# Performance work log

Measured on AMD Instinct MI355X. Metric: run time of the kernel, lower is better.

Reference implementation:

```python
import jax, jax.numpy as jnp
import numpy as np

ANGLE_DEG = 15.0  # matches init_kwargs angle; cv2 convention: positive = counter-clockwise


def setup_inputs() -> dict:
    key = jax.random.key(0)
    encode_image = jax.random.normal(key, (32, 3, 512, 512), dtype=jnp.float32)
    return {"encode_image": encode_image}


def _rotate(img, angle_deg):
    """Faithful jax version of cv2.getRotationMatrix2D + cv2.warpAffine
    (INTER_LINEAR, BORDER_CONSTANT=0, scale=1), batched over B,C.
    cv2.warpAffine inverts M, so dst(x,y) = src(R(-angle) @ (x-c, y-c) + c).
    """
    B, C, H, W = img.shape
    theta = jnp.float32(angle_deg * np.pi / 180.0)
    a, b = jnp.cos(theta), jnp.sin(theta)
    # original code uses center (H//2, W//2) with dsize (H, W); square images assumed
    cx = jnp.float32(H // 2)
    cy = jnp.float32(W // 2)
    X, Y = jnp.meshgrid(jnp.arange(W, dtype=jnp.float32),
                        jnp.arange(H, dtype=jnp.float32))  # [H, W] dst pixel coords
    # inverse rotation (R(angle)^-1 = R(-angle)) about center
    xs = a * (X - cx) - b * (Y - cy) + cx  # src column coord
    ys = b * (X - cx) + a * (Y - cy) + cy  # src row coord
    x0 = jnp.floor(xs)
    y0 = jnp.floor(ys)
    wx = xs - x0
    wy = ys - y0
    x0i = x0.astype(jnp.int32)
    y0i = y0.astype(jnp.int32)

    def tap(yi, xi, w):
        # per-tap border-constant-0 handling, as cv2 BORDER_CONSTANT does
        valid = (xi >= 0) & (xi <= W - 1) & (yi >= 0) & (yi <= H - 1)
        xc = jnp.clip(xi, 0, W - 1)
        yc = jnp.clip(yi, 0, H - 1)
        vals = img[:, :, yc, xc]  # gather -> [B, C, H, W]
        return vals * (w * valid)[None, None]

    out = (tap(y0i,     x0i,     (1 - wy) * (1 - wx))
         + tap(y0i,     x0i + 1, (1 - wy) * wx)
         + tap(y0i + 1, x0i,     wy * (1 - wx))
         + tap(y0i + 1, x0i + 1, wy * wx))
    return out


def reference(encode_image):
    return _rotate(encode_image, ANGLE_DEG)
```

## Files before the change

### kernel.cpp

```cpp
#include <hip/hip_runtime.h>


#define IMG_H 512
#define IMG_W 512
#define NPLANES 96
#define TSX 64
#define TSY 32
#define LROWS 50
#define LCOLS 76
#define GPR 19
#define NGROUPS_PAD 1024
#define LDS_FLOATS (NGROUPS_PAD * 4)

typedef __attribute__((address_space(1))) const float gfloat;
typedef __attribute__((address_space(3))) float sfloat;

template <bool MASKED>
__device__ __forceinline__ void compute_tile(const float* __restrict__ tile,
                                             float* __restrict__ dst,
                                             int X0, int Y0, int xs0a, int ys0,
                                             int t, float a, float b) {
    const int col4 = (t & 15) << 2;
    const int row_base = t >> 4;
#pragma unroll
    for (int rr = 0; rr < 2; ++rr) {
        const int y = Y0 + row_base + (rr << 4);
        const float fy = (float)y - 256.0f;
        const float bxs = -b * fy + 256.0f;
        const float bys =  a * fy + 256.0f;

        float o[4];
#pragma unroll
        for (int k = 0; k < 4; ++k) {
            const int x = X0 + col4 + k;
            const float fx = (float)x - 256.0f;
            const float xs = a * fx + bxs;
            const float ys = b * fx + bys;

            const float x0f = floorf(xs);
            const float y0f = floorf(ys);
            const float wx = xs - x0f;
            const float wy = ys - y0f;
            const int x0 = (int)x0f;
            const int y0 = (int)y0f;

            float w00 = (1.0f - wy) * (1.0f - wx);
            float w01 = (1.0f - wy) * wx;
            float w10 = wy * (1.0f - wx);
            float w11 = wy * wx;

            if (MASKED) {
                const float vx0 = ((unsigned)x0       < IMG_W) ? 1.0f : 0.0f;
                const float vx1 = ((unsigned)(x0 + 1) < IMG_W) ? 1.0f : 0.0f;
                const float vy0 = ((unsigned)y0       < IMG_H) ? 1.0f : 0.0f;
                const float vy1 = ((unsigned)(y0 + 1) < IMG_H) ? 1.0f : 0.0f;
                w00 *= vy0 * vx0;
                w01 *= vy0 * vx1;
                w10 *= vy1 * vx0;
                w11 *= vy1 * vx1;
            }

            const int lr = y0 - ys0;
            const int lc = x0 - xs0a;
            const float* __restrict__ p = &tile[lr * LCOLS + lc];
            const float v00 = p[0];
            const float v01 = p[1];
            const float v10 = p[LCOLS];
            const float v11 = p[LCOLS + 1];

            o[k] = v00 * w00 + v01 * w01 + v10 * w10 + v11 * w11;
        }
        *reinterpret_cast<float4*>(&dst[y * IMG_W + X0 + col4]) =
            make_float4(o[0], o[1], o[2], o[3]);
    }
}

__global__ __launch_bounds__(256, 8) void rot_kernel(const float* __restrict__ in,
                                                     float* __restrict__ out) {
    const float a = 0.96592582628906831f;
    const float b = 0.25881904510252074f;

    __shared__ float tile[LDS_FLOATS];

    const int blk = blockIdx.x;
    const int tx = blk & 7;
    const int ty = (blk >> 3) & 15;
    const int bc = blk >> 7;
    const int X0 = tx * TSX;
    const int Y0 = ty * TSY;

    const float fx_lo = (float)X0 - 256.0f;
    const float fy_lo = (float)Y0 - 256.0f;
    const float fy_hi = (float)(Y0 + (TSY - 1)) - 256.0f;
    const float xs_min = a * fx_lo + (-b * fy_hi + 256.0f);
    const float ys_min = b * fx_lo + ( a * fy_lo + 256.0f);
    const int xs0  = (int)floorf(xs_min);
    const int ys0  = (int)floorf(ys_min);
    const int xs0a = xs0 & ~3;

    const int t = threadIdx.x;
    const int wave = t >> 6;
    const int plane_base = bc * (IMG_H * IMG_W);
    const int total = NPLANES * IMG_H * IMG_W;

#pragma unroll
    for (int it = 0; it < NGROUPS_PAD / 256; ++it) {
        const int g = it * 256 + t;
        const int r = g / GPR;
        const int c4 = (g - r * GPR) << 2;
        int gidx = plane_base + (ys0 + r) * IMG_W + xs0a + c4;
        gidx = min(max(gidx, 0), total - 4);
        __builtin_amdgcn_global_load_lds(
            (gfloat*)(in + gidx),
            (sfloat*)&tile[(it * 256 + (wave << 6)) * 4],
            16, 0, 0);
    }
    __syncthreads();

    float* __restrict__ dst = out + (size_t)bc * (IMG_H * IMG_W);

    const bool interior = (xs0a >= 0) && (xs0a + LCOLS <= IMG_W) &&
                          (ys0 >= 0) && (ys0 + LROWS <= IMG_H);
    if (interior) {
        compute_tile<false>(tile, dst, X0, Y0, xs0a, ys0, t, a, b);
    } else {
        compute_tile<true>(tile, dst, X0, Y0, xs0a, ys0, t, a, b);
    }
}

extern "C" void kernel_launch(void* const* d_in, const int* in_sizes, int n_in,
                              void* d_out, int out_size, void* d_ws, size_t ws_size,
                              hipStream_t stream) {
    const float* in = (const float*)d_in[0];
    float* out = (float*)d_out;

    const int grid = NPLANES * (IMG_W / TSX) * (IMG_H / TSY);
    rot_kernel<<<grid, 256, 0, stream>>>(in, out);
}
```

Before: 174.0 us.

## Persistent blocks with double-buffered LDS prefetch of next tile

Replaces one-tile-per-block launch with 1024 persistent blocks that each process 12 consecutive tiles. The next tile's source window is loaded into a second LDS buffer with async global_load_lds while the current tile is computed, hiding load latency. Occupancy hint drops to 4 blocks/SM and LDS use doubles, which may reduce latency hiding across blocks. The __syncthreads before the store is relied on for the loads to complete, with no explicit wait on the async copies.

```diff
diff --git a/kernel.cpp b/kernel.cpp
--- a/kernel.cpp
+++ b/kernel.cpp
@@ -9,22 +9,46 @@
 #define LROWS 50
 #define LCOLS 76
 #define GPR 19
-#define NGROUPS_PAD 1024
-#define LDS_FLOATS (NGROUPS_PAD * 4)
+#define BUF_FLOATS 4096
+#define NBLOCKS 1024
+#define TPB 12
 
 typedef __attribute__((address_space(1))) const float gfloat;
 typedef __attribute__((address_space(3))) float sfloat;
 
+struct TileGeom {
+    int X0, Y0, xs0a, ys0, bc;
+    bool interior;
+};
+
+__device__ __forceinline__ TileGeom decode(int tl, float a, float b) {
+    TileGeom g;
+    g.bc = tl >> 7;
+    const int rem = tl & 127;
+    g.X0 = (rem & 7) * TSX;
+    g.Y0 = (rem >> 3) * TSY;
+    const float fx_lo = (float)g.X0 - 256.0f;
+    const float fy_lo = (float)g.Y0 - 256.0f;
+    const float fy_hi = (float)(g.Y0 + TSY - 1) - 256.0f;
+    const float xs_min = a * fx_lo + (-b * fy_hi + 256.0f);
+    const float ys_min = b * fx_lo + ( a * fy_lo + 256.0f);
+    const int xs0 = (int)floorf(xs_min);
+    g.ys0 = (int)floorf(ys_min);
+    g.xs0a = xs0 & ~3;
+    g.interior = (g.xs0a >= 0) && (g.xs0a + LCOLS <= IMG_W) &&
+                 (g.ys0 >= 0) && (g.ys0 + LROWS <= IMG_H);
+    return g;
+}
+
 template <bool MASKED>
-__device__ __forceinline__ void compute_tile(const float* __restrict__ tile,
-                                             float* __restrict__ dst,
-                                             int X0, int Y0, int xs0a, int ys0,
-                                             int t, float a, float b) {
+__device__ __forceinline__ void compute_px(const float* __restrict__ buf,
+                                           const TileGeom& G, int t,
+                                           float a, float b, float4 res[2]) {
     const int col4 = (t & 15) << 2;
     const int row_base = t >> 4;
 #pragma unroll
     for (int rr = 0; rr < 2; ++rr) {
-        const int y = Y0 + row_base + (rr << 4);
+        const int y = G.Y0 + row_base + (rr << 4);
         const float fy = (float)y - 256.0f;
         const float bxs = -b * fy + 256.0f;
         const float bys =  a * fy + 256.0f;
@@ -32,7 +56,7 @@
         float o[4];
 #pragma unroll
         for (int k = 0; k < 4; ++k) {
-            const int x = X0 + col4 + k;
+            const int x = G.X0 + col4 + k;
             const float fx = (float)x - 256.0f;
             const float xs = a * fx + bxs;
             const float ys = b * fx + bys;
@@ -60,9 +84,9 @@
                 w11 *= vy1 * vx1;
             }
 
-            const int lr = y0 - ys0;
-            const int lc = x0 - xs0a;
-            const float* __restrict__ p = &tile[lr * LCOLS + lc];
+            const int lr = y0 - G.ys0;
+            const int lc = x0 - G.xs0a;
+            const float* __restrict__ p = &buf[lr * LCOLS + lc];
             const float v00 = p[0];
             const float v01 = p[1];
             const float v10 = p[LCOLS];
@@ -70,61 +94,77 @@
 
             o[k] = v00 * w00 + v01 * w01 + v10 * w10 + v11 * w11;
         }
-        *reinterpret_cast<float4*>(&dst[y * IMG_W + X0 + col4]) =
-            make_float4(o[0], o[1], o[2], o[3]);
+        res[rr] = make_float4(o[0], o[1], o[2], o[3]);
     }
 }
 
-__global__ __launch_bounds__(256, 8) void rot_kernel(const float* __restrict__ in,
+__device__ __forceinline__ void store_px(float* __restrict__ out,
+                                         const TileGeom& G, int t,
+                                         const float4 res[2]) {
+    const int col4 = (t & 15) << 2;
+    const int row_base = t >> 4;
+    float* __restrict__ dst = out + (size_t)G.bc * (IMG_H * IMG_W);
+#pragma unroll
+    for (int rr = 0; rr < 2; ++rr) {
+        const int y = G.Y0 + row_base + (rr << 4);
+        *reinterpret_cast<float4*>(&dst[y * IMG_W + G.X0 + col4]) = res[rr];
+    }
+}
+
+__global__ __launch_bounds__(256, 4) void rot_kernel(const float* __restrict__ in,
                                                      float* __restrict__ out) {
     const float a = 0.96592582628906831f;
     const float b = 0.25881904510252074f;
 
-    __shared__ float tile[LDS_FLOATS];
-
-    const int blk = blockIdx.x;
-    const int tx = blk & 7;
-    const int ty = (blk >> 3) & 15;
-    const int bc = blk >> 7;
-    const int X0 = tx * TSX;
-    const int Y0 = ty * TSY;
-
-    const float fx_lo = (float)X0 - 256.0f;
-    const float fy_lo = (float)Y0 - 256.0f;
-    const float fy_hi = (float)(Y0 + (TSY - 1)) - 256.0f;
-    const float xs_min = a * fx_lo + (-b * fy_hi + 256.0f);
-    const float ys_min = b * fx_lo + ( a * fy_lo + 256.0f);
-    const int xs0  = (int)floorf(xs_min);
-    const int ys0  = (int)floorf(ys_min);
-    const int xs0a = xs0 & ~3;
+    __shared__ float tile[2][BUF_FLOATS];
 
     const int t = threadIdx.x;
     const int wave = t >> 6;
-    const int plane_base = bc * (IMG_H * IMG_W);
     const int total = NPLANES * IMG_H * IMG_W;
 
+    int gof[4], ldso[4];
 #pragma unroll
-    for (int it = 0; it < NGROUPS_PAD / 256; ++it) {
+    for (int it = 0; it < 4; ++it) {
         const int g = it * 256 + t;
         const int r = g / GPR;
         const int c4 = (g - r * GPR) << 2;
-        int gidx = plane_base + (ys0 + r) * IMG_W + xs0a + c4;
-        gidx = min(max(gidx, 0), total - 4);
-        __builtin_amdgcn_global_load_lds(
-            (gfloat*)(in + gidx),
-            (sfloat*)&tile[(it * 256 + (wave << 6)) * 4],
-            16, 0, 0);
+        gof[it] = r * IMG_W + c4;
+        ldso[it] = (it * 256 + (wave << 6)) * 4;
     }
+
+    auto stage = [&](const TileGeom& G, int p) {
+        const int base = G.bc * (IMG_H * IMG_W) + G.ys0 * IMG_W + G.xs0a;
+#pragma unroll
+        for (int it = 0; it < 4; ++it) {
+            int gidx = base + gof[it];
+            gidx = min(max(gidx, 0), total - 4);
+            __builtin_amdgcn_global_load_lds(
+                (gfloat*)(in + gidx), (sfloat*)&tile[p][ldso[it]], 16, 0, 0);
+        }
+    };
+
+    const int tile0 = blockIdx.x * TPB;
+
+    TileGeom G = decode(tile0, a, b);
+    stage(G, 0);
     __syncthreads();
 
-    float* __restrict__ dst = out + (size_t)bc * (IMG_H * IMG_W);
-
-    const bool interior = (xs0a >= 0) && (xs0a + LCOLS <= IMG_W) &&
-                          (ys0 >= 0) && (ys0 + LROWS <= IMG_H);
-    if (interior) {
-        compute_tile<false>(tile, dst, X0, Y0, xs0a, ys0, t, a, b);
-    } else {
-        compute_tile<true>(tile, dst, X0, Y0, xs0a, ys0, t, a, b);
+    float4 res[2];
+#pragma unroll 2
+    for (int i = 0; i < TPB; ++i) {
+        const int p = i & 1;
+        TileGeom Gn;
+        if (i + 1 < TPB) {
+            Gn = decode(tile0 + i + 1, a, b);
+            stage(Gn, p ^ 1);
+        }
+        if (G.interior)
+            compute_px<false>(&tile[p][0], G, t, a, b, res);
+        else
+            compute_px<true>(&tile[p][0], G, t, a, b, res);
+        __syncthreads();
+        store_px(out, G, t, res);
+        G = Gn;
     }
 }
 
@@ -133,7 +173,5 @@
                               hipStream_t stream) {
     const float* in = (const float*)d_in[0];
     float* out = (float*)d_out;
-
-    const int grid = NPLANES * (IMG_W / TSX) * (IMG_H / TSY);
-    rot_kernel<<<grid, 256, 0, stream>>>(in, out);
+    rot_kernel<<<NBLOCKS, 256, 0, stream>>>(in, out);
 }
```

Result: slower. 191.4 us (+9.9%).
